# Performance work log

Hardware: AMD Instinct MI355X
Metric: run time of the kernel (lower is better)

Reference implementation:

```python
import jax, jax.numpy as jnp
import numpy as np

N, C, H = 4096, 768, 12
HD = C // H
SCALE = HD ** -0.5


def setup_inputs() -> dict:
    key = jax.random.key(0)
    k1, k2, k3 = jax.random.split(key, 3)
    x = jax.random.normal(k1, (N, C), dtype=jnp.float32)
    w_qkv = jax.random.normal(k2, (C, 3 * C), dtype=jnp.float32) * (C ** -0.5)
    w_proj = jax.random.normal(k3, (C, C), dtype=jnp.float32) * (C ** -0.5)
    b_proj = jnp.zeros((C,), dtype=jnp.float32)
    return {"x": x, "w_qkv": w_qkv, "w_proj": w_proj, "b_proj": b_proj}


def reference(x, w_qkv, w_proj, b_proj):
    n, c = x.shape
    # fused QKV projection (qkv_bias=False): [N, 3C] -> [3, H, N, hd]
    qkv = (x @ w_qkv).reshape(n, 3, H, HD)
    qkv = jnp.transpose(qkv, (1, 2, 0, 3))  # (3, H, N, hd)
    q, k, v = qkv[0], qkv[1], qkv[2]
    # scaled dot-product attention per head: (H, N, N)
    attn = jnp.einsum('hnd,hmd->hnm', q, k) * SCALE
    attn = jax.nn.softmax(attn, axis=-1)
    # attn_drop is identity (rate=0, eval mode)
    out = jnp.einsum('hnm,hmd->hnd', attn, v)          # (H, N, hd)
    out = jnp.transpose(out, (1, 0, 2)).reshape(n, c)  # (N, C)
    # output projection (bias by default in nn.Dense); proj_drop identity
    return out @ w_proj + b_proj
```

## Files before the change

### kernel.cpp

```cpp
#include <hip/hip_runtime.h>

#define N_TOK 4096
#define C_DIM 768
#define H_NUM 12
#define QKV_N 2304

typedef __attribute__((ext_vector_type(8))) short bf16x8;
typedef __attribute__((ext_vector_type(4))) float f32x4;
typedef __attribute__((ext_vector_type(16))) float f32x16;
typedef __attribute__((ext_vector_type(4))) unsigned int u32x4;

static __device__ __forceinline__ unsigned short f2bf(float f) {
  unsigned u = __builtin_bit_cast(unsigned, f);
  u += 0x7FFF + ((u >> 16) & 1);
  return (unsigned short)(u >> 16);
}

static __device__ __forceinline__ float bf2f(unsigned short u) {
  return __builtin_bit_cast(float, (unsigned)u << 16);
}

static __device__ __forceinline__ float exp2_fast(float x) {
  float r; asm("v_exp_f32 %0, %1" : "=v"(r) : "v"(x)); return r;
}

#define GLOAD_LDS16(g, l)                                                     \
  __builtin_amdgcn_global_load_lds(                                           \
      (const __attribute__((address_space(1))) void*)(g),                     \
      (__attribute__((address_space(3))) void*)(l), 16, 0, 0)

#define Q_SCALE 0.18033688011112042f

__global__ __launch_bounds__(256) void prep_fused(
    const float* __restrict__ wq, unsigned short* __restrict__ wqT,
    const float* __restrict__ x, unsigned short* __restrict__ xb) {
  __shared__ unsigned short T[64][65];
  const int t = threadIdx.x;
  if (blockIdx.x < 432) {
    const int tid = blockIdx.x;
    const int n0 = (tid % 36) * 64, k0 = (tid / 36) * 64;
    {
      const int r = t >> 2, qd = t & 3;
#pragma unroll
      for (int i = 0; i < 4; ++i) {
        const int c = qd * 16 + i * 4;
        const float4 v = *reinterpret_cast<const float4*>(
            &wq[(size_t)(k0 + r) * QKV_N + n0 + c]);
        T[r][c + 0] = f2bf(v.x); T[r][c + 1] = f2bf(v.y);
        T[r][c + 2] = f2bf(v.z); T[r][c + 3] = f2bf(v.w);
      }
    }
    __syncthreads();
#pragma unroll
    for (int i = 0; i < 2; ++i) {
      const int cid = t + i * 256;
      const int rn = cid >> 3, cx = cid & 7;
      unsigned short tmp[8];
#pragma unroll
      for (int j = 0; j < 8; ++j) tmp[j] = T[cx * 8 + j][rn];
      *reinterpret_cast<bf16x8*>(&wqT[(size_t)(n0 + rn) * 768 + k0 + cx * 8]) =
          *reinterpret_cast<bf16x8*>(tmp);
    }
  } else {
    const int i = (blockIdx.x - 432) * 256 + t;
    const float4 a = reinterpret_cast<const float4*>(x)[i * 2];
    const float4 b = reinterpret_cast<const float4*>(x)[i * 2 + 1];
    unsigned short tmp[8] = {f2bf(a.x), f2bf(a.y), f2bf(a.z), f2bf(a.w),
                             f2bf(b.x), f2bf(b.y), f2bf(b.z), f2bf(b.w)};
    reinterpret_cast<bf16x8*>(xb)[i] = *reinterpret_cast<bf16x8*>(tmp);
  }
}

__global__ __launch_bounds__(256) void transpose_cvt(
    const float* __restrict__ in, unsigned short* __restrict__ out,
    int K, int N) {
  __shared__ unsigned short T[64][65];
  const int t = threadIdx.x;
  const int k0 = blockIdx.y * 64, n0 = blockIdx.x * 64;
  {
    const int r = t >> 2, qd = t & 3;
#pragma unroll
    for (int i = 0; i < 4; ++i) {
      const int c = qd * 16 + i * 4;
      const float4 v = *reinterpret_cast<const float4*>(
          &in[(size_t)(k0 + r) * N + n0 + c]);
      T[r][c + 0] = f2bf(v.x); T[r][c + 1] = f2bf(v.y);
      T[r][c + 2] = f2bf(v.z); T[r][c + 3] = f2bf(v.w);
    }
  }
  __syncthreads();
#pragma unroll
  for (int i = 0; i < 2; ++i) {
    const int cid = t + i * 256;
    const int rn = cid >> 3, cx = cid & 7;
    unsigned short tmp[8];
#pragma unroll
    for (int j = 0; j < 8; ++j) tmp[j] = T[cx * 8 + j][rn];
    *reinterpret_cast<bf16x8*>(&out[(size_t)(n0 + rn) * K + k0 + cx * 8]) =
        *reinterpret_cast<bf16x8*>(tmp);
  }
}

__global__ __launch_bounds__(256) void gemm_qkv_bf16(
    const unsigned short* __restrict__ A, const unsigned short* __restrict__ Bt,
    unsigned short* __restrict__ qw, unsigned short* __restrict__ kw,
    unsigned short* __restrict__ vw) {
  __shared__ unsigned short As[128 * 32];
  __shared__ unsigned short Bs[128 * 32];
  const int t = threadIdx.x;
  const int lane = t & 63, wid = t >> 6;
  const int lr = lane & 15, lg = lane >> 4;
  const int lid = blockIdx.y * 18 + blockIdx.x;
  const int swz = (lid & 7) * 72 + (lid >> 3);
  const int m_base = (swz / 18) * 128, n_base = (swz % 18) * 128;
  const int wm = (wid >> 1) * 64, wn = (wid & 1) * 64;
  const int c_row = lane >> 2;
  const int c_col = (lane & 3) * 8;

  f32x4 acc[4][4];
#pragma unroll
  for (int mt = 0; mt < 4; ++mt)
#pragma unroll
    for (int nt = 0; nt < 4; ++nt) acc[mt][nt] = (f32x4){0.f, 0.f, 0.f, 0.f};

  for (int kt = 0; kt < 24; ++kt) {
    const int k0 = kt * 32;
    __syncthreads();
#pragma unroll
    for (int i = 0; i < 2; ++i) {
      const int ch = wid * 2 + i;
      GLOAD_LDS16(&A[(size_t)(m_base + ch * 16 + c_row) * 768 + k0 + c_col],
                  &As[ch * 512]);
      GLOAD_LDS16(&Bt[(size_t)(n_base + ch * 16 + c_row) * 768 + k0 + c_col],
                  &Bs[ch * 512]);
    }
    __syncthreads();
    bf16x8 af[4], bfr[4];
#pragma unroll
    for (int mt = 0; mt < 4; ++mt)
      af[mt] = *reinterpret_cast<const bf16x8*>(&As[(wm + mt * 16 + lr) * 32 + lg * 8]);
#pragma unroll
    for (int nt = 0; nt < 4; ++nt)
      bfr[nt] = *reinterpret_cast<const bf16x8*>(&Bs[(wn + nt * 16 + lr) * 32 + lg * 8]);
#pragma unroll
    for (int mt = 0; mt < 4; ++mt)
#pragma unroll
      for (int nt = 0; nt < 4; ++nt)
        acc[mt][nt] = __builtin_amdgcn_mfma_f32_16x16x32_bf16(af[mt], bfr[nt],
                                                              acc[mt][nt], 0, 0, 0);
  }
#pragma unroll
  for (int mt = 0; mt < 4; ++mt)
#pragma unroll
    for (int nt = 0; nt < 4; ++nt)
#pragma unroll
      for (int r = 0; r < 4; ++r) {
        const int m = m_base + wm + mt * 16 + lg * 4 + r;
        const int c = n_base + wn + nt * 16 + lr;
        const float v = acc[mt][nt][r];
        const int which = c / 768;
        const int cc = c - which * 768;
        const int h = cc >> 6, d = cc & 63;
        if (which == 0) {
          qw[((size_t)h * N_TOK + m) * 64 + d] = f2bf(v * Q_SCALE);
        } else if (which == 1) {
          kw[((size_t)h * N_TOK + m) * 64 + d] = f2bf(v);
        } else {
          vw[((size_t)h * 64 + d) * N_TOK + m] = f2bf(v);
        }
      }
}

__global__ __launch_bounds__(256) void gemm_proj_bf16(
    const unsigned short* __restrict__ A, const unsigned short* __restrict__ Bt,
    const float* __restrict__ bias, float* __restrict__ out) {
  __shared__ unsigned short As[128 * 32];
  __shared__ unsigned short Bs[128 * 32];
  const int t = threadIdx.x;
  const int lane = t & 63, wid = t >> 6;
  const int lr = lane & 15, lg = lane >> 4;
  const int lid = blockIdx.y * 6 + blockIdx.x;
  const int swz = (lid & 7) * 24 + (lid >> 3);
  const int m_base = (swz / 6) * 128, n_base = (swz % 6) * 128;
  const int wm = (wid >> 1) * 64, wn = (wid & 1) * 64;
  const int c_row = lane >> 2;
  const int c_col = (lane & 3) * 8;

  f32x4 acc[4][4];
#pragma unroll
  for (int mt = 0; mt < 4; ++mt)
#pragma unroll
    for (int nt = 0; nt < 4; ++nt) acc[mt][nt] = (f32x4){0.f, 0.f, 0.f, 0.f};

  for (int kt = 0; kt < 24; ++kt) {
    const int k0 = kt * 32;
    __syncthreads();
#pragma unroll
    for (int i = 0; i < 2; ++i) {
      const int ch = wid * 2 + i;
      GLOAD_LDS16(&A[(size_t)(m_base + ch * 16 + c_row) * 768 + k0 + c_col],
                  &As[ch * 512]);
      GLOAD_LDS16(&Bt[(size_t)(n_base + ch * 16 + c_row) * 768 + k0 + c_col],
                  &Bs[ch * 512]);
    }
    __syncthreads();
    bf16x8 af[4], bfr[4];
#pragma unroll
    for (int mt = 0; mt < 4; ++mt)
      af[mt] = *reinterpret_cast<const bf16x8*>(&As[(wm + mt * 16 + lr) * 32 + lg * 8]);
#pragma unroll
    for (int nt = 0; nt < 4; ++nt)
      bfr[nt] = *reinterpret_cast<const bf16x8*>(&Bs[(wn + nt * 16 + lr) * 32 + lg * 8]);
#pragma unroll
    for (int mt = 0; mt < 4; ++mt)
#pragma unroll
      for (int nt = 0; nt < 4; ++nt)
        acc[mt][nt] = __builtin_amdgcn_mfma_f32_16x16x32_bf16(af[mt], bfr[nt],
                                                              acc[mt][nt], 0, 0, 0);
  }
#pragma unroll
  for (int nt = 0; nt < 4; ++nt) {
    const int n = n_base + wn + nt * 16 + lr;
    const float bv = bias[n];
#pragma unroll
    for (int mt = 0; mt < 4; ++mt)
#pragma unroll
      for (int r = 0; r < 4; ++r) {
        const int m = m_base + wm + mt * 16 + lg * 4 + r;
        out[(size_t)m * 768 + n] = acc[mt][nt][r] + bv;
      }
  }
}

__global__ __launch_bounds__(256) void attn_kernel(
    const unsigned short* __restrict__ qw, const unsigned short* __restrict__ kw,
    const unsigned short* __restrict__ vw, unsigned short* __restrict__ po0,
    unsigned short* __restrict__ po1, float* __restrict__ lw) {
  __shared__ unsigned short smem[16384];
  const int t = threadIdx.x;
  const int lane = t & 63;
  const int qsub = t >> 6;
  const int q31 = lane & 31;
  const int hi = lane >> 5;
  const int q7 = q31 & 7;
  const int swz = (blockIdx.x & 7) * 96 + (blockIdx.x >> 3);
  const int h = swz >> 6;
  const int rem = swz & 63;
  const int half = rem >> 5;
  const int qst = rem & 31;
  const int q0 = qst * 128 + qsub * 32;

  const unsigned short* kbase = &kw[(size_t)h * N_TOK * 64];
  const unsigned short* vbase = &vw[(size_t)h * 64 * N_TOK];
  const int kv0 = half * 2048;

  const int lr8 = lane >> 3;
  const int lc8 = lane & 7;
  const int sck = lc8 ^ lr8;

  bf16x8 qf[4];
#pragma unroll
  for (int ks = 0; ks < 4; ++ks)
    qf[ks] = *reinterpret_cast<const bf16x8*>(
        &qw[((size_t)h * N_TOK + q0 + q31) * 64 + ks * 16 + hi * 8]);

  f32x16 acc0, acc1;
#pragma unroll
  for (int r = 0; r < 16; ++r) { acc0[r] = 0.f; acc1[r] = 0.f; }
  float l_run = 0.f;

#pragma unroll
  for (int i = 0; i < 2; ++i) {
    const int rowblk = (qsub * 2 + i) * 8;
    GLOAD_LDS16(&kbase[(size_t)(kv0 + rowblk + lr8) * 64 + sck * 8],
                &smem[rowblk * 64]);
    GLOAD_LDS16(&vbase[(size_t)(rowblk + lr8) * N_TOK + kv0 + sck * 8],
                &smem[4096 + rowblk * 64]);
  }

  int cur = 0;
  for (int kvt = 0; kvt < 32; ++kvt) {
    asm volatile("s_waitcnt vmcnt(0)" ::: "memory");
    __syncthreads();
    if (kvt + 1 < 32) {
      const int kvn = kv0 + (kvt + 1) * 64;
      unsigned short* nb = &smem[(cur ^ 1) * 8192];
#pragma unroll
      for (int i = 0; i < 2; ++i) {
        const int rowblk = (qsub * 2 + i) * 8;
        GLOAD_LDS16(&kbase[(size_t)(kvn + rowblk + lr8) * 64 + sck * 8],
                    &nb[rowblk * 64]);
        GLOAD_LDS16(&vbase[(size_t)(rowblk + lr8) * N_TOK + kvn + sck * 8],
                    &nb[4096 + rowblk * 64]);
      }
    }
    const unsigned short* Ks = &smem[cur * 8192];
    const unsigned short* Vs = Ks + 4096;
    cur ^= 1;

#pragma unroll
    for (int ct = 0; ct < 2; ++ct) {
      f32x16 s;
#pragma unroll
      for (int r = 0; r < 16; ++r) s[r] = 0.f;
      __builtin_amdgcn_s_setprio(1);
#pragma unroll
      for (int ks = 0; ks < 4; ++ks) {
        const bf16x8 kf = *reinterpret_cast<const bf16x8*>(
            &Ks[(ct * 32 + q31) * 64 + (((ks * 2 + hi) ^ q7) << 3)]);
        s = __builtin_amdgcn_mfma_f32_32x32x16_bf16(kf, qf[ks], s, 0, 0, 0);
      }
      __builtin_amdgcn_s_setprio(0);

      float p[16];
#pragma unroll
      for (int r = 0; r < 16; ++r) p[r] = exp2_fast(s[r]);
      float s8[8];
#pragma unroll
      for (int r = 0; r < 8; ++r) s8[r] = p[r] + p[r + 8];
#pragma unroll
      for (int r = 0; r < 4; ++r) s8[r] = s8[r] + s8[r + 4];
      l_run += (s8[0] + s8[1]) + (s8[2] + s8[3]);

      unsigned dw[8];
#pragma unroll
      for (int m2 = 0; m2 < 8; ++m2)
        asm("v_cvt_pk_bf16_f32 %0, %1, %2"
            : "=v"(dw[m2]) : "v"(p[2 * m2]), "v"(p[2 * m2 + 1]));
      asm("v_permlane32_swap_b32 %0, %1" : "+v"(dw[0]), "+v"(dw[2]));
      asm("v_permlane32_swap_b32 %0, %1" : "+v"(dw[1]), "+v"(dw[3]));
      asm("v_permlane32_swap_b32 %0, %1" : "+v"(dw[4]), "+v"(dw[6]));
      asm("v_permlane32_swap_b32 %0, %1" : "+v"(dw[5]), "+v"(dw[7]));

      __builtin_amdgcn_s_setprio(1);
#pragma unroll
      for (int ksl = 0; ksl < 2; ++ksl) {
        u32x4 u;
        u.x = dw[ksl * 4 + 0]; u.y = dw[ksl * 4 + 1];
        u.z = dw[ksl * 4 + 2]; u.w = dw[ksl * 4 + 3];
        const bf16x8 pa = __builtin_bit_cast(bf16x8, u);
        const int kg = ct * 2 + ksl;
        const int vchk = ((kg * 2 + hi) ^ q7) << 3;
        const bf16x8 vf0 = *reinterpret_cast<const bf16x8*>(
            &Vs[q31 * 64 + vchk]);
        const bf16x8 vf1 = *reinterpret_cast<const bf16x8*>(
            &Vs[(32 + q31) * 64 + vchk]);
        acc0 = __builtin_amdgcn_mfma_f32_32x32x16_bf16(pa, vf0, acc0, 0, 0, 0);
        acc1 = __builtin_amdgcn_mfma_f32_32x32x16_bf16(pa, vf1, acc1, 0, 0, 0);
      }
      __builtin_amdgcn_s_setprio(0);
    }
  }

  l_run += __shfl_xor(l_run, 32);
  const float linv = 1.0f / l_run;
  unsigned short* pout = half ? po1 : po0;
#pragma unroll
  for (int r = 0; r < 16; ++r) {
    const int crow = (r & 3) + 8 * (r >> 2) + 4 * hi;
    const float iv = __shfl(linv, crow);
    const size_t base = (size_t)(q0 + crow) * C_DIM + h * 64;
    pout[base + q31] = f2bf(acc0[r] * iv);
    pout[base + 32 + q31] = f2bf(acc1[r] * iv);
  }
  if (hi == 0) lw[half * 49152 + h * 4096 + q0 + q31] = l_run;
}

__global__ __launch_bounds__(256) void attn_merge(
    unsigned short* __restrict__ po0, const unsigned short* __restrict__ po1,
    const float* __restrict__ lw) {
  const int i = blockIdx.x * 256 + threadIdx.x;
  const int base = i * 8;
  const int q = base / 768;
  const int c = base - q * 768;
  const int h = c >> 6;
  const float l0 = lw[h * 4096 + q];
  const float l1 = lw[49152 + h * 4096 + q];
  const float w = 1.0f / (l0 + l1);
  const float w0 = l0 * w, w1 = l1 * w;
  const bf16x8 a = *reinterpret_cast<const bf16x8*>(&po0[base]);
  const bf16x8 b = *reinterpret_cast<const bf16x8*>(&po1[base]);
  unsigned short tmp[8];
#pragma unroll
  for (int j = 0; j < 8; ++j)
    tmp[j] = f2bf(w0 * bf2f((unsigned short)a[j]) +
                  w1 * bf2f((unsigned short)b[j]));
  *reinterpret_cast<bf16x8*>(&po0[base]) = *reinterpret_cast<bf16x8*>(tmp);
}

extern "C" void kernel_launch(void* const* d_in, const int* in_sizes, int n_in,
                              void* d_out, int out_size, void* d_ws, size_t ws_size,
                              hipStream_t stream) {
  (void)in_sizes; (void)n_in; (void)out_size; (void)ws_size;
  const float* x = (const float*)d_in[0];
  const float* w_qkv = (const float*)d_in[1];
  const float* w_proj = (const float*)d_in[2];
  const float* b_proj = (const float*)d_in[3];
  float* out = (float*)d_out;

  const size_t HNd = (size_t)H_NUM * N_TOK * 64;
  unsigned short* qw = (unsigned short*)d_ws;
  unsigned short* kw = qw + HNd;
  unsigned short* vw = kw + HNd;
  unsigned short* xb = vw + HNd;
  unsigned short* ow = xb;
  unsigned short* wT = xb + HNd;
  unsigned short* wqkvT = wT;
  unsigned short* wprojT = wT;
  unsigned short* po1 = wT + HNd;
  float* lw = (float*)(po1 + HNd);

  prep_fused<<<dim3(1968), 256, 0, stream>>>(w_qkv, wqkvT, x, xb);
  gemm_qkv_bf16<<<dim3(QKV_N / 128, N_TOK / 128), 256, 0, stream>>>(
      xb, wqkvT, qw, kw, vw);
  transpose_cvt<<<dim3(C_DIM / 64, C_DIM / 64), 256, 0, stream>>>(
      w_proj, wprojT, C_DIM, C_DIM);
  attn_kernel<<<dim3(768), 256, 0, stream>>>(qw, kw, vw, ow, po1, lw);
  attn_merge<<<dim3(N_TOK * C_DIM / 8 / 256), 256, 0, stream>>>(ow, po1, lw);
  gemm_proj_bf16<<<dim3(C_DIM / 128, N_TOK / 128), 256, 0, stream>>>(
      ow, wprojT, b_proj, out);
}
```

Before: 139.1 us.

## Double-buffer LDS in both GEMMs and fold w_proj transpose into prep kernel

Both bf16 GEMMs now keep two LDS stages, so the global-to-LDS load for the next k-tile is issued before the MFMA work on the current tile. This leaves one barrier per iteration instead of two and overlaps memory latency with compute. Separately, the w_proj transpose/convert is merged into the prep_fused launch, which removes one kernel launch. It also places wprojT at its own workspace offset so it no longer aliases wqkvT. LDS use per block doubles, which may reduce occupancy.

```diff
diff --git a/kernel.cpp b/kernel.cpp
--- a/kernel.cpp
+++ b/kernel.cpp
@@ -33,19 +33,28 @@
 
 __global__ __launch_bounds__(256) void prep_fused(
     const float* __restrict__ wq, unsigned short* __restrict__ wqT,
+    const float* __restrict__ wp, unsigned short* __restrict__ wpT,
     const float* __restrict__ x, unsigned short* __restrict__ xb) {
   __shared__ unsigned short T[64][65];
   const int t = threadIdx.x;
-  if (blockIdx.x < 432) {
-    const int tid = blockIdx.x;
-    const int n0 = (tid % 36) * 64, k0 = (tid / 36) * 64;
+  if (blockIdx.x < 576) {
+    const float* in; unsigned short* outp; int N, n0, k0;
+    if (blockIdx.x < 432) {
+      const int tid = blockIdx.x;
+      in = wq; outp = wqT; N = QKV_N;
+      n0 = (tid % 36) * 64; k0 = (tid / 36) * 64;
+    } else {
+      const int tid = blockIdx.x - 432;
+      in = wp; outp = wpT; N = C_DIM;
+      n0 = (tid % 12) * 64; k0 = (tid / 12) * 64;
+    }
     {
       const int r = t >> 2, qd = t & 3;
 #pragma unroll
       for (int i = 0; i < 4; ++i) {
         const int c = qd * 16 + i * 4;
         const float4 v = *reinterpret_cast<const float4*>(
-            &wq[(size_t)(k0 + r) * QKV_N + n0 + c]);
+            &in[(size_t)(k0 + r) * N + n0 + c]);
         T[r][c + 0] = f2bf(v.x); T[r][c + 1] = f2bf(v.y);
         T[r][c + 2] = f2bf(v.z); T[r][c + 3] = f2bf(v.w);
       }
@@ -58,11 +67,11 @@
       unsigned short tmp[8];
 #pragma unroll
       for (int j = 0; j < 8; ++j) tmp[j] = T[cx * 8 + j][rn];
-      *reinterpret_cast<bf16x8*>(&wqT[(size_t)(n0 + rn) * 768 + k0 + cx * 8]) =
+      *reinterpret_cast<bf16x8*>(&outp[(size_t)(n0 + rn) * 768 + k0 + cx * 8]) =
           *reinterpret_cast<bf16x8*>(tmp);
     }
   } else {
-    const int i = (blockIdx.x - 432) * 256 + t;
+    const int i = (blockIdx.x - 576) * 256 + t;
     const float4 a = reinterpret_cast<const float4*>(x)[i * 2];
     const float4 b = reinterpret_cast<const float4*>(x)[i * 2 + 1];
     unsigned short tmp[8] = {f2bf(a.x), f2bf(a.y), f2bf(a.z), f2bf(a.w),
@@ -71,42 +80,12 @@
   }
 }
 
-__global__ __launch_bounds__(256) void transpose_cvt(
-    const float* __restrict__ in, unsigned short* __restrict__ out,
-    int K, int N) {
-  __shared__ unsigned short T[64][65];
-  const int t = threadIdx.x;
-  const int k0 = blockIdx.y * 64, n0 = blockIdx.x * 64;
-  {
-    const int r = t >> 2, qd = t & 3;
-#pragma unroll
-    for (int i = 0; i < 4; ++i) {
-      const int c = qd * 16 + i * 4;
-      const float4 v = *reinterpret_cast<const float4*>(
-          &in[(size_t)(k0 + r) * N + n0 + c]);
-      T[r][c + 0] = f2bf(v.x); T[r][c + 1] = f2bf(v.y);
-      T[r][c + 2] = f2bf(v.z); T[r][c + 3] = f2bf(v.w);
-    }
-  }
-  __syncthreads();
-#pragma unroll
-  for (int i = 0; i < 2; ++i) {
-    const int cid = t + i * 256;
-    const int rn = cid >> 3, cx = cid & 7;
-    unsigned short tmp[8];
-#pragma unroll
-    for (int j = 0; j < 8; ++j) tmp[j] = T[cx * 8 + j][rn];
-    *reinterpret_cast<bf16x8*>(&out[(size_t)(n0 + rn) * K + k0 + cx * 8]) =
-        *reinterpret_cast<bf16x8*>(tmp);
-  }
-}
-
 __global__ __launch_bounds__(256) void gemm_qkv_bf16(
     const unsigned short* __restrict__ A, const unsigned short* __restrict__ Bt,
     unsigned short* __restrict__ qw, unsigned short* __restrict__ kw,
     unsigned short* __restrict__ vw) {
-  __shared__ unsigned short As[128 * 32];
-  __shared__ unsigned short Bs[128 * 32];
+  __shared__ unsigned short As[2][128 * 32];
+  __shared__ unsigned short Bs[2][128 * 32];
   const int t = threadIdx.x;
   const int lane = t & 63, wid = t >> 6;
   const int lr = lane & 15, lg = lane >> 4;
@@ -123,31 +102,46 @@
 #pragma unroll
     for (int nt = 0; nt < 4; ++nt) acc[mt][nt] = (f32x4){0.f, 0.f, 0.f, 0.f};
 
+#pragma unroll
+  for (int i = 0; i < 2; ++i) {
+    const int ch = wid * 2 + i;
+    GLOAD_LDS16(&A[(size_t)(m_base + ch * 16 + c_row) * 768 + c_col],
+                &As[0][ch * 512]);
+    GLOAD_LDS16(&Bt[(size_t)(n_base + ch * 16 + c_row) * 768 + c_col],
+                &Bs[0][ch * 512]);
+  }
+
+  int cur = 0;
   for (int kt = 0; kt < 24; ++kt) {
-    const int k0 = kt * 32;
+    asm volatile("s_waitcnt vmcnt(0)" ::: "memory");
     __syncthreads();
-#pragma unroll
-    for (int i = 0; i < 2; ++i) {
-      const int ch = wid * 2 + i;
-      GLOAD_LDS16(&A[(size_t)(m_base + ch * 16 + c_row) * 768 + k0 + c_col],
-                  &As[ch * 512]);
-      GLOAD_LDS16(&Bt[(size_t)(n_base + ch * 16 + c_row) * 768 + k0 + c_col],
-                  &Bs[ch * 512]);
-    }
-    __syncthreads();
+    if (kt + 1 < 24) {
+      const int k0n = (kt + 1) * 32;
+#pragma unroll
+      for (int i = 0; i < 2; ++i) {
+        const int ch = wid * 2 + i;
+        GLOAD_LDS16(&A[(size_t)(m_base + ch * 16 + c_row) * 768 + k0n + c_col],
+                    &As[cur ^ 1][ch * 512]);
+        GLOAD_LDS16(&Bt[(size_t)(n_base + ch * 16 + c_row) * 768 + k0n + c_col],
+                    &Bs[cur ^ 1][ch * 512]);
+      }
+    }
     bf16x8 af[4], bfr[4];
 #pragma unroll
     for (int mt = 0; mt < 4; ++mt)
-      af[mt] = *reinterpret_cast<const bf16x8*>(&As[(wm + mt * 16 + lr) * 32 + lg * 8]);
+      af[mt] = *reinterpret_cast<const bf16x8*>(
+          &As[cur][(wm + mt * 16 + lr) * 32 + lg * 8]);
 #pragma unroll
     for (int nt = 0; nt < 4; ++nt)
-      bfr[nt] = *reinterpret_cast<const bf16x8*>(&Bs[(wn + nt * 16 + lr) * 32 + lg * 8]);
+      bfr[nt] = *reinterpret_cast<const bf16x8*>(
+          &Bs[cur][(wn + nt * 16 + lr) * 32 + lg * 8]);
 #pragma unroll
     for (int mt = 0; mt < 4; ++mt)
 #pragma unroll
       for (int nt = 0; nt < 4; ++nt)
         acc[mt][nt] = __builtin_amdgcn_mfma_f32_16x16x32_bf16(af[mt], bfr[nt],
                                                               acc[mt][nt], 0, 0, 0);
+    cur ^= 1;
   }
 #pragma unroll
   for (int mt = 0; mt < 4; ++mt)
@@ -174,8 +168,8 @@
 __global__ __launch_bounds__(256) void gemm_proj_bf16(
     const unsigned short* __restrict__ A, const unsigned short* __restrict__ Bt,
     const float* __restrict__ bias, float* __restrict__ out) {
-  __shared__ unsigned short As[128 * 32];
-  __shared__ unsigned short Bs[128 * 32];
+  __shared__ unsigned short As[2][128 * 32];
+  __shared__ unsigned short Bs[2][128 * 32];
   const int t = threadIdx.x;
   const int lane = t & 63, wid = t >> 6;
   const int lr = lane & 15, lg = lane >> 4;
@@ -192,31 +186,46 @@
 #pragma unroll
     for (int nt = 0; nt < 4; ++nt) acc[mt][nt] = (f32x4){0.f, 0.f, 0.f, 0.f};
 
+#pragma unroll
+  for (int i = 0; i < 2; ++i) {
+    const int ch = wid * 2 + i;
+    GLOAD_LDS16(&A[(size_t)(m_base + ch * 16 + c_row) * 768 + c_col],
+                &As[0][ch * 512]);
+    GLOAD_LDS16(&Bt[(size_t)(n_base + ch * 16 + c_row) * 768 + c_col],
+                &Bs[0][ch * 512]);
+  }
+
+  int cur = 0;
   for (int kt = 0; kt < 24; ++kt) {
-    const int k0 = kt * 32;
+    asm volatile("s_waitcnt vmcnt(0)" ::: "memory");
     __syncthreads();
-#pragma unroll
-    for (int i = 0; i < 2; ++i) {
-      const int ch = wid * 2 + i;
-      GLOAD_LDS16(&A[(size_t)(m_base + ch * 16 + c_row) * 768 + k0 + c_col],
-                  &As[ch * 512]);
-      GLOAD_LDS16(&Bt[(size_t)(n_base + ch * 16 + c_row) * 768 + k0 + c_col],
-                  &Bs[ch * 512]);
-    }
-    __syncthreads();
+    if (kt + 1 < 24) {
+      const int k0n = (kt + 1) * 32;
+#pragma unroll
+      for (int i = 0; i < 2; ++i) {
+        const int ch = wid * 2 + i;
+        GLOAD_LDS16(&A[(size_t)(m_base + ch * 16 + c_row) * 768 + k0n + c_col],
+                    &As[cur ^ 1][ch * 512]);
+        GLOAD_LDS16(&Bt[(size_t)(n_base + ch * 16 + c_row) * 768 + k0n + c_col],
+                    &Bs[cur ^ 1][ch * 512]);
+      }
+    }
     bf16x8 af[4], bfr[4];
 #pragma unroll
     for (int mt = 0; mt < 4; ++mt)
-      af[mt] = *reinterpret_cast<const bf16x8*>(&As[(wm + mt * 16 + lr) * 32 + lg * 8]);
+      af[mt] = *reinterpret_cast<const bf16x8*>(
+          &As[cur][(wm + mt * 16 + lr) * 32 + lg * 8]);
 #pragma unroll
     for (int nt = 0; nt < 4; ++nt)
-      bfr[nt] = *reinterpret_cast<const bf16x8*>(&Bs[(wn + nt * 16 + lr) * 32 + lg * 8]);
+      bfr[nt] = *reinterpret_cast<const bf16x8*>(
+          &Bs[cur][(wn + nt * 16 + lr) * 32 + lg * 8]);
 #pragma unroll
     for (int mt = 0; mt < 4; ++mt)
 #pragma unroll
       for (int nt = 0; nt < 4; ++nt)
         acc[mt][nt] = __builtin_amdgcn_mfma_f32_16x16x32_bf16(af[mt], bfr[nt],
                                                               acc[mt][nt], 0, 0, 0);
+    cur ^= 1;
   }
 #pragma unroll
   for (int nt = 0; nt < 4; ++nt) {
@@ -406,15 +415,13 @@
   unsigned short* ow = xb;
   unsigned short* wT = xb + HNd;
   unsigned short* wqkvT = wT;
-  unsigned short* wprojT = wT;
+  unsigned short* wprojT = wT + 1769472;
   unsigned short* po1 = wT + HNd;
   float* lw = (float*)(po1 + HNd);
 
-  prep_fused<<<dim3(1968), 256, 0, stream>>>(w_qkv, wqkvT, x, xb);
+  prep_fused<<<dim3(2112), 256, 0, stream>>>(w_qkv, wqkvT, w_proj, wprojT, x, xb);
   gemm_qkv_bf16<<<dim3(QKV_N / 128, N_TOK / 128), 256, 0, stream>>>(
       xb, wqkvT, qw, kw, vw);
-  transpose_cvt<<<dim3(C_DIM / 64, C_DIM / 64), 256, 0, stream>>>(
-      w_proj, wprojT, C_DIM, C_DIM);
   attn_kernel<<<dim3(768), 256, 0, stream>>>(qw, kw, vw, ow, po1, lw);
   attn_merge<<<dim3(N_TOK * C_DIM / 8 / 256), 256, 0, stream>>>(ow, po1, lw);
   gemm_proj_bf16<<<dim3(C_DIM / 128, N_TOK / 128), 256, 0, stream>>>(
```

Result: slower. 142.5 us (+2.5%).
